# Kernel tuning notes

Measured on AMD Instinct MI355X. Metric: run time of the kernel, lower is better.

## Reference

```python
import jax, jax.numpy as jnp
import numpy as np

DIM_MODEL = 1024
DIM_K = 64
DIM_V = 64
H = 16
B = 2
S = 2048


def setup_inputs() -> dict:
    key = jax.random.key(0)
    ks = jax.random.split(key, 11)
    s = 0.02
    return {
        "Q": jax.random.normal(ks[0], (B, S, DIM_MODEL), jnp.float32),
        "K": jax.random.normal(ks[1], (B, S, DIM_MODEL), jnp.float32),
        "V": jax.random.normal(ks[2], (B, S, DIM_MODEL), jnp.float32),
        "Wq": jax.random.normal(ks[3], (DIM_MODEL, H * DIM_K), jnp.float32) * s,
        "bq": jnp.zeros((H * DIM_K,), jnp.float32),
        "Wk": jax.random.normal(ks[4], (DIM_MODEL, H * DIM_K), jnp.float32) * s,
        "bk": jnp.zeros((H * DIM_K,), jnp.float32),
        "Wv": jax.random.normal(ks[5], (DIM_MODEL, H * DIM_V), jnp.float32) * s,
        "bv": jnp.zeros((H * DIM_V,), jnp.float32),
        "Wo": jax.random.normal(ks[6], (H * DIM_V, DIM_MODEL), jnp.float32) * s,
        "bo": jnp.zeros((DIM_MODEL,), jnp.float32),
    }


def reference(Q, K, V, Wq, bq, Wk, bk, Wv, bv, Wo, bo):
    b, len_q = Q.shape[0], Q.shape[1]
    # QKV projections, split heads: [b, h, S, d]
    q = (Q @ Wq + bq).reshape(b, len_q, H, DIM_K).transpose(0, 2, 1, 3)
    k = (K @ Wk + bk).reshape(b, K.shape[1], H, DIM_K).transpose(0, 2, 1, 3)
    v = (V @ Wv + bv).reshape(b, V.shape[1], H, DIM_V).transpose(0, 2, 1, 3)
    # FAITHFUL QUIRK: original scales by sqrt(K.shape[0]) == batch size, not dim_k
    scale = 1.0 / np.sqrt(b).astype(np.float32)
    att = jnp.einsum('bhqd,bhkd->bhqk', q * scale, k)
    att = jax.nn.softmax(att, axis=-1)
    out = jnp.einsum('bhqk,bhkd->bhqd', att, v)  # [b,h,S,dv]
    out = out.transpose(0, 2, 1, 3).reshape(b, len_q, H * DIM_V)
    return out @ Wo + bo
```

## Files before the change

### kernel.cpp

```cpp
#include <hip/hip_runtime.h>
#include <hip/hip_bf16.h>


using bf16 = __hip_bfloat16;
typedef __attribute__((ext_vector_type(4))) float f32x4;
typedef __attribute__((ext_vector_type(8))) short bf16x8;

__device__ __forceinline__ void gload_lds16(const void* gsrc, void* ldst) {
    __builtin_amdgcn_global_load_lds(
        (const __attribute__((address_space(1))) void*)gsrc,
        (__attribute__((address_space(3))) void*)ldst,
        16, 0, 0);
}

__device__ __forceinline__ float fexp2(float x) {
    float r; asm("v_exp_f32 %0, %1" : "=v"(r) : "v"(x)); return r;
}

__device__ __forceinline__ unsigned cvtpk(float a, float b) {
    unsigned d; asm("v_cvt_pk_bf16_f32 %0, %1, %2" : "=v"(d) : "v"(a), "v"(b));
    return d;
}

__device__ __forceinline__ void pls32(unsigned &a, unsigned &b) {
    asm("v_permlane32_swap_b32 %0, %1" : "+v"(a), "+v"(b));
}
__device__ __forceinline__ void pls16(unsigned &a, unsigned &b) {
    asm("v_permlane16_swap_b32 %0, %1" : "+v"(a), "+v"(b));
}

__device__ __forceinline__ unsigned pack2bf(float a, float b) {
    unsigned short ua = __builtin_bit_cast(unsigned short, __float2bfloat16(a));
    unsigned short ub = __builtin_bit_cast(unsigned short, __float2bfloat16(b));
    return (unsigned)ua | ((unsigned)ub << 16);
}

__global__ void prep_kernel(const float* __restrict__ X0, const float* __restrict__ X1,
                            const float* __restrict__ X2,
                            bf16* __restrict__ O0, bf16* __restrict__ O1, bf16* __restrict__ O2,
                            const float* __restrict__ W0, const float* __restrict__ W1,
                            const float* __restrict__ W2, const float* __restrict__ W3,
                            bf16* __restrict__ T0, bf16* __restrict__ T1,
                            bf16* __restrict__ T2, bf16* __restrict__ T3,
                            int n4) {
    const int z = blockIdx.z;
    if (z < 3) {
        const float* in = z == 0 ? X0 : (z == 1 ? X1 : X2);
        bf16* out = z == 0 ? O0 : (z == 1 ? O1 : O2);
        int idx = blockIdx.x * blockDim.x + threadIdx.x;
        int stride = gridDim.x * blockDim.x;
        for (int i = idx; i < n4; i += stride) {
            float4 v = reinterpret_cast<const float4*>(in)[i];
            reinterpret_cast<uint2*>(out)[i] = make_uint2(pack2bf(v.x, v.y), pack2bf(v.z, v.w));
        }
    } else {
        const int w = z - 3;
        const float* W = w == 0 ? W0 : (w == 1 ? W1 : (w == 2 ? W2 : W3));
        bf16* WT = w == 0 ? T0 : (w == 1 ? T1 : (w == 2 ? T2 : T3));
        __shared__ float t[32][33];
        int bx = (blockIdx.x & 31) * 32, by = (blockIdx.x >> 5) * 32;
        int x = threadIdx.x & 31, y = threadIdx.x >> 5;
        #pragma unroll
        for (int i = 0; i < 4; ++i)
            t[y + 8*i][x] = W[(size_t)(by + y + 8*i) * 1024 + bx + x];
        __syncthreads();
        #pragma unroll
        for (int i = 0; i < 4; ++i)
            WT[(size_t)(bx + y + 8*i) * 1024 + by + x] = __float2bfloat16(t[x][y + 8*i]);
    }
}

template<int NTILE>
__global__ __launch_bounds__(256, (NTILE == 128) ? 2 : 3)
void gemm_bt(const bf16* __restrict__ A0, const bf16* __restrict__ A1, const bf16* __restrict__ A2,
             const bf16* __restrict__ B0, const bf16* __restrict__ B1, const bf16* __restrict__ B2,
             const float* __restrict__ bi0, const float* __restrict__ bi1, const float* __restrict__ bi2,
             void* __restrict__ O0, void* __restrict__ O1, void* __restrict__ O2,
             int mode_base)
{
    const int f = blockIdx.x;
    int x, y, z;
    if (NTILE == 128) {
        const int s = f >> 3;
        y = s & 7;
        const int t = (f & 7) + 8 * (s >> 3);
        x = t & 31; z = t >> 5;
    } else {
        const int s = f >> 3;
        y = s & 15;
        x = (f & 7) + 8 * (s >> 4);
        z = 0;
    }
    const bf16* A  = z == 0 ? A0 : (z == 1 ? A1 : A2);
    const bf16* BT = z == 0 ? B0 : (z == 1 ? B1 : B2);
    const float* bias = z == 0 ? bi0 : (z == 1 ? bi1 : bi2);
    void* Cout = z == 0 ? O0 : (z == 1 ? O1 : O2);
    const int mode = mode_base + z;

    constexpr int ABYTES = 16384;
    constexpr int BBYTES = NTILE * 128;
    constexpr int BUFB   = ABYTES + BBYTES;
    __shared__ __align__(16) char Sbuf[2 * BUFB];
    constexpr int MF = (NTILE == 128) ? 4 : 2;
    const int tid = threadIdx.x;
    const int wave = tid >> 6, lane = tid & 63;
    const int g = lane >> 4, ln = lane & 15;
    const int m0 = x * 128, n0 = y * NTILE;
    const int wm = (NTILE == 128) ? (wave >> 1) * 64 : wave * 32;
    const int wn = (NTILE == 128) ? (wave & 1) * 64 : 0;
    const int lnsw = (ln & 7) << 4;

    auto stage = [&](int k0, int buf) {
        char* Ab = Sbuf + buf * BUFB;
        char* Bb = Ab + ABYTES;
        #pragma unroll
        for (int rd = 0; rd < 4; ++rd) {
            int row = rd * 32 + (tid >> 3);
            int src = ((tid & 7) * 16) ^ (((tid >> 3) & 7) << 4);
            gload_lds16((const char*)(A + (size_t)(m0 + row) * 1024 + k0) + src,
                        Ab + rd * 4096 + tid * 16);
        }
        #pragma unroll
        for (int rd = 0; rd < NTILE / 32; ++rd) {
            int row = rd * 32 + (tid >> 3);
            int src = ((tid & 7) * 16) ^ (((tid >> 3) & 7) << 4);
            gload_lds16((const char*)(BT + (size_t)(n0 + row) * 1024 + k0) + src,
                        Bb + rd * 4096 + tid * 16);
        }
    };

    f32x4 acc[MF][4] = {};
    stage(0, 0);

    for (int k = 0; k < 16; ++k) {
        const int cur = k & 1;
        asm volatile("s_waitcnt vmcnt(0)\n\ts_barrier" ::: "memory");
        __builtin_amdgcn_sched_barrier(0);
        if (k < 15) stage((k + 1) * 64, cur ^ 1);
        __builtin_amdgcn_sched_barrier(0);

        const char* Ab = Sbuf + cur * BUFB;
        const char* Bb = Ab + ABYTES;
        #pragma unroll
        for (int kk = 0; kk < 2; ++kk) {
            bf16x8 af[MF], bfr[4];
            #pragma unroll
            for (int mf = 0; mf < MF; ++mf)
                af[mf] = *(const bf16x8*)(Ab + (wm + mf*16 + ln) * 128 + ((kk*64 + g*16) ^ lnsw));
            #pragma unroll
            for (int nf = 0; nf < 4; ++nf)
                bfr[nf] = *(const bf16x8*)(Bb + (wn + nf*16 + ln) * 128 + ((kk*64 + g*16) ^ lnsw));
            #pragma unroll
            for (int mf = 0; mf < MF; ++mf)
                #pragma unroll
                for (int nf = 0; nf < 4; ++nf)
                    acc[mf][nf] = __builtin_amdgcn_mfma_f32_16x16x32_bf16(af[mf], bfr[nf], acc[mf][nf], 0, 0, 0);
        }
    }

    const float scl = (mode == 0) ? (0.70710678118654752f * 1.44269504088896340f) : 1.0f;

    if (mode == 2) {
        #pragma unroll
        for (int mf = 0; mf < MF; ++mf) {
            #pragma unroll
            for (int nf = 0; nf < 4; ++nf) {
                int col = n0 + wn + nf*16 + ln;
                float bv = bias[col];
                int row0 = m0 + wm + mf*16 + g*4;
                int b = row0 >> 11, ss = row0 & 2047;
                int hh = col >> 6, dv = col & 63;
                bf16* dst = (bf16*)Cout + (((size_t)(b*16 + hh) * 64 + dv) << 11) + ss;
                *(uint2*)dst = make_uint2(
                    pack2bf(acc[mf][nf][0] + bv, acc[mf][nf][1] + bv),
                    pack2bf(acc[mf][nf][2] + bv, acc[mf][nf][3] + bv));
            }
        }
    } else if (mode == 0 || mode == 1) {
        __syncthreads();
        #pragma unroll
        for (int mf = 0; mf < MF; ++mf) {
            #pragma unroll
            for (int nf = 0; nf < 4; ++nf) {
                int tcol = wn + nf*16 + ln;
                float bv = bias[n0 + tcol];
                #pragma unroll
                for (int r = 0; r < 4; ++r) {
                    int trow = wm + mf*16 + g*4 + r;
                    *(unsigned short*)(Sbuf + trow * (NTILE*2) + tcol * 2) =
                        __builtin_bit_cast(unsigned short,
                            __float2bfloat16((acc[mf][nf][r] + bv) * scl));
                }
            }
        }
        __syncthreads();
        constexpr int TPR = NTILE / 8;
        const int rr = tid / TPR, cc = (tid % TPR) * 8;
        #pragma unroll
        for (int it = 0; it < 128 / (256 / TPR); ++it) {
            int row = it * (256 / TPR) + rr;
            uint4 v = *(const uint4*)(Sbuf + row * (NTILE*2) + cc * 2);
            *(uint4*)((bf16*)Cout + (size_t)(m0 + row) * 1024 + n0 + cc) = v;
        }
    } else {
        #pragma unroll
        for (int p = 0; p < 2; ++p) {
            __syncthreads();
            #pragma unroll
            for (int mf = 0; mf < MF; ++mf) {
                #pragma unroll
                for (int j = 0; j < 2; ++j) {
                    int nf = p * 2 + j;
                    int tcol = j*16 + ln;
                    float bv = bias[n0 + wn + nf*16 + ln];
                    #pragma unroll
                    for (int r = 0; r < 4; ++r) {
                        int trow = wm + mf*16 + g*4 + r;
                        *(float*)(Sbuf + trow * 128 + tcol * 4) = acc[mf][nf][r] + bv;
                    }
                }
            }
            __syncthreads();
            const int rr = tid >> 3, cc = (tid & 7) * 4;
            #pragma unroll
            for (int it = 0; it < 4; ++it) {
                int row = it * 32 + rr;
                uint4 v = *(const uint4*)(Sbuf + row * 128 + cc * 4);
                *(uint4*)((float*)Cout + (size_t)(m0 + row) * 1024 + n0 + p*32 + cc) = v;
            }
        }
    }
}

__global__ __launch_bounds__(256, 2)
void attn_kernel(const bf16* __restrict__ qh, const bf16* __restrict__ kh,
                 const bf16* __restrict__ vt, bf16* __restrict__ aout)
{
    __shared__ __align__(16) bf16 Kls[2][128 * 64];
    __shared__ __align__(16) bf16 Vls[2][64 * 128];
    const int f = blockIdx.x;
    const int xcd = f & 7, s = f >> 3, i = s & 15, ghi = s >> 4;
    const int bh = xcd + 8 * ghi;
    const int b = bh >> 4, h = bh & 15;
    const int q0 = i * 128;

    const int tid = threadIdx.x;
    const int wave = tid >> 6, lane = tid & 63;
    const int g = lane >> 4, ln = lane & 15;
    const int srow = lane >> 3;
    const int scol = ((lane & 7) * 16) ^ ((srow & 7) << 4);
    const int lnsw = (ln & 7) << 4;

    const bf16* kbase = kh + (size_t)(b * 2048) * 1024 + h * 64;
    const bf16* vbase = vt + (size_t)bh * 64 * 2048;

    const int vrow_in = lane >> 4;
    const int vcol16 = lane & 15;

    bf16x8 qf[2][2];
    #pragma unroll
    for (int nf = 0; nf < 2; ++nf) {
        const bf16* qrow = qh + (size_t)(b*2048 + q0 + wave*32 + nf*16 + ln) * 1024 + h*64;
        qf[nf][0] = *(const bf16x8*)(qrow + g*8);
        qf[nf][1] = *(const bf16x8*)(qrow + 32 + g*8);
    }

    auto stageKV = [&](int kv0, int buf) {
        #pragma unroll
        for (int c2 = 0; c2 < 4; ++c2) {
            int c = wave * 4 + c2;
            int krow = c * 8 + srow;
            gload_lds16((const char*)(kbase + (size_t)(kv0 + krow) * 1024) + scol,
                        (char*)&Kls[buf][0] + c * 1024);
        }
        #pragma unroll
        for (int c2 = 0; c2 < 4; ++c2) {
            int c = wave * 4 + c2;
            int vrow = c * 4 + vrow_in;
            int sc16 = vcol16 ^ (vrow & 15);
            gload_lds16((const char*)(vbase + (size_t)vrow * 2048 + kv0) + sc16 * 16,
                        (char*)&Vls[buf][0] + c * 1024);
        }
    };

    stageKV(0, 0);

    f32x4 oacc[4][2] = {};
    f32x4 lacc[2] = {};
    union PU { unsigned u[4]; bf16x8 v; };
    PU ones;
    ones.u[0] = ones.u[1] = ones.u[2] = ones.u[3] = 0x3F803F80u;

    for (int t = 0; t < 16; ++t) {
        const int cur = t & 1;
        asm volatile("s_waitcnt vmcnt(0)\n\ts_barrier" ::: "memory");
        __builtin_amdgcn_sched_barrier(0);
        if (t < 15) stageKV((t + 1) * 128, cur ^ 1);
        __builtin_amdgcn_sched_barrier(0);

        const char* Kc = (const char*)&Kls[cur][0];
        const char* Vc = (const char*)&Vls[cur][0];

        f32x4 sacA[4][2] = {}, sacB[4][2] = {};
        __builtin_amdgcn_s_setprio(1);
        #pragma unroll
        for (int kk = 0; kk < 2; ++kk) {
            bf16x8 kf[4];
            #pragma unroll
            for (int mf = 0; mf < 4; ++mf)
                kf[mf] = *(const bf16x8*)(Kc + (mf*16 + ln) * 128 + ((kk*64 + g*16) ^ lnsw));
            #pragma unroll
            for (int mf = 0; mf < 4; ++mf)
                #pragma unroll
                for (int nf = 0; nf < 2; ++nf)
                    sacA[mf][nf] = __builtin_amdgcn_mfma_f32_16x16x32_bf16(kf[mf], qf[nf][kk], sacA[mf][nf], 0, 0, 0);
        }
        #pragma unroll
        for (int kk = 0; kk < 2; ++kk) {
            bf16x8 kf[4];
            #pragma unroll
            for (int mf = 0; mf < 4; ++mf)
                kf[mf] = *(const bf16x8*)(Kc + (64 + mf*16 + ln) * 128 + ((kk*64 + g*16) ^ lnsw));
            #pragma unroll
            for (int mf = 0; mf < 4; ++mf)
                #pragma unroll
                for (int nf = 0; nf < 2; ++nf)
                    sacB[mf][nf] = __builtin_amdgcn_mfma_f32_16x16x32_bf16(kf[mf], qf[nf][kk], sacB[mf][nf], 0, 0, 0);
        }
        __builtin_amdgcn_s_setprio(0);

        PU pfh[2][2][2];
        #pragma unroll
        for (int ha = 0; ha < 2; ++ha) {
            f32x4 (&sac)[4][2] = ha ? sacB : sacA;
            #pragma unroll
            for (int nf = 0; nf < 2; ++nf) {
                unsigned w[4][2];
                #pragma unroll
                for (int mf = 0; mf < 4; ++mf) {
                    float e0 = fexp2(sac[mf][nf][0]);
                    float e1 = fexp2(sac[mf][nf][1]);
                    float e2 = fexp2(sac[mf][nf][2]);
                    float e3 = fexp2(sac[mf][nf][3]);
                    w[mf][0] = cvtpk(e0, e1);
                    w[mf][1] = cvtpk(e2, e3);
                }
                #pragma unroll
                for (int kk = 0; kk < 2; ++kk) {
                    #pragma unroll
                    for (int rp = 0; rp < 2; ++rp) {
                        unsigned a = w[2*kk][rp], bb = w[2*kk + 1][rp];
                        pls32(a, bb);
                        pls16(a, bb);
                        pfh[ha][nf][kk].u[rp] = a;
                        pfh[ha][nf][kk].u[2 + rp] = bb;
                    }
                }
            }
        }

        __builtin_amdgcn_s_setprio(1);
        #pragma unroll
        for (int ha = 0; ha < 2; ++ha) {
            #pragma unroll
            for (int kk = 0; kk < 2; ++kk) {
                bf16x8 vf[4];
                #pragma unroll
                for (int mf = 0; mf < 4; ++mf)
                    vf[mf] = *(const bf16x8*)(Vc + (mf*16 + ln) * 256 + (((ha*8 + kk*4 + g) ^ ln) << 4));
                #pragma unroll
                for (int nf = 0; nf < 2; ++nf)
                    lacc[nf] = __builtin_amdgcn_mfma_f32_16x16x32_bf16(ones.v, pfh[ha][nf][kk].v, lacc[nf], 0, 0, 0);
                #pragma unroll
                for (int mf = 0; mf < 4; ++mf)
                    #pragma unroll
                    for (int nf = 0; nf < 2; ++nf)
                        oacc[mf][nf] = __builtin_amdgcn_mfma_f32_16x16x32_bf16(vf[mf], pfh[ha][nf][kk].v, oacc[mf][nf], 0, 0, 0);
            }
        }
        __builtin_amdgcn_s_setprio(0);
    }

    #pragma unroll
    for (int nf = 0; nf < 2; ++nf) {
        float inv = 1.0f / lacc[nf][0];
        int q = q0 + wave*32 + nf*16 + ln;
        bf16* orow = aout + (size_t)(b*2048 + q) * 1024 + h * 64;
        #pragma unroll
        for (int mf = 0; mf < 4; ++mf) {
            *(uint2*)(orow + mf*16 + g*4) = make_uint2(
                pack2bf(oacc[mf][nf][0] * inv, oacc[mf][nf][1] * inv),
                pack2bf(oacc[mf][nf][2] * inv, oacc[mf][nf][3] * inv));
        }
    }
}

extern "C" void kernel_launch(void* const* d_in, const int* in_sizes, int n_in,
                              void* d_out, int out_size, void* d_ws, size_t ws_size,
                              hipStream_t stream)
{
    const float* Q  = (const float*)d_in[0];
    const float* K  = (const float*)d_in[1];
    const float* V  = (const float*)d_in[2];
    const float* Wq = (const float*)d_in[3];
    const float* bq = (const float*)d_in[4];
    const float* Wk = (const float*)d_in[5];
    const float* bk = (const float*)d_in[6];
    const float* Wv = (const float*)d_in[7];
    const float* bv = (const float*)d_in[8];
    const float* Wo = (const float*)d_in[9];
    const float* bo = (const float*)d_in[10];

    char* ws = (char*)d_ws;
    const size_t MB = 1024 * 1024;
    bf16* Qbf  = (bf16*)(ws + 0);
    bf16* Kbf  = (bf16*)(ws + 8*MB);
    bf16* Vbf  = (bf16*)(ws + 16*MB);
    bf16* WqT  = (bf16*)(ws + 24*MB);
    bf16* WkT  = (bf16*)(ws + 26*MB);
    bf16* WvT  = (bf16*)(ws + 28*MB);
    bf16* WoT  = (bf16*)(ws + 30*MB);
    bf16* qhp  = (bf16*)(ws + 32*MB);
    bf16* khp  = (bf16*)(ws + 40*MB);
    bf16* vtp  = (bf16*)(ws + 48*MB);
    bf16* aout = (bf16*)(ws + 0);

    const int n4 = (2 * 2048 * 1024) / 4;
    prep_kernel<<<dim3(1024, 1, 7), 256, 0, stream>>>(Q, K, V, Qbf, Kbf, Vbf,
                                                      Wq, Wk, Wv, Wo, WqT, WkT, WvT, WoT, n4);

    gemm_bt<128><<<768, 256, 0, stream>>>(Qbf, Kbf, Vbf, WqT, WkT, WvT,
                                          bq, bk, bv, qhp, khp, vtp, 0);

    attn_kernel<<<512, 256, 0, stream>>>(qhp, khp, vtp, aout);

    gemm_bt<64><<<512, 256, 0, stream>>>(aout, aout, aout, WoT, WoT, WoT,
                                         bo, bo, bo, d_out, d_out, d_out, 3);
}
```

Before: 104.4 us.

## Load V fragments directly from global into registers instead of LDS staging

Drops the double-buffered V tile in LDS. Each wave now reads its V MFMA operands straight from global memory into registers at the start of every KV iteration, issued before the next K tile is staged. This halves LDS use, which may allow more blocks per CU, and removes the LDS reads for V. In exchange every wave re-fetches the same V tile from global/L2 with no sharing across waves. The loads are not prefetched a tile ahead, so their latency can sit on the critical path, and the vmcnt(0) wait also covers them. Register pressure rises by 16 bf16x8 values per lane.

```diff
diff --git a/kernel.cpp b/kernel.cpp
--- a/kernel.cpp
+++ b/kernel.cpp
@@ -237,7 +237,6 @@
                  const bf16* __restrict__ vt, bf16* __restrict__ aout)
 {
     __shared__ __align__(16) bf16 Kls[2][128 * 64];
-    __shared__ __align__(16) bf16 Vls[2][64 * 128];
     const int f = blockIdx.x;
     const int xcd = f & 7, s = f >> 3, i = s & 15, ghi = s >> 4;
     const int bh = xcd + 8 * ghi;
@@ -254,9 +253,6 @@
     const bf16* kbase = kh + (size_t)(b * 2048) * 1024 + h * 64;
     const bf16* vbase = vt + (size_t)bh * 64 * 2048;
 
-    const int vrow_in = lane >> 4;
-    const int vcol16 = lane & 15;
-
     bf16x8 qf[2][2];
     #pragma unroll
     for (int nf = 0; nf < 2; ++nf) {
@@ -265,7 +261,7 @@
         qf[nf][1] = *(const bf16x8*)(qrow + 32 + g*8);
     }
 
-    auto stageKV = [&](int kv0, int buf) {
+    auto stageK = [&](int kv0, int buf) {
         #pragma unroll
         for (int c2 = 0; c2 < 4; ++c2) {
             int c = wave * 4 + c2;
@@ -273,17 +269,9 @@
             gload_lds16((const char*)(kbase + (size_t)(kv0 + krow) * 1024) + scol,
                         (char*)&Kls[buf][0] + c * 1024);
         }
-        #pragma unroll
-        for (int c2 = 0; c2 < 4; ++c2) {
-            int c = wave * 4 + c2;
-            int vrow = c * 4 + vrow_in;
-            int sc16 = vcol16 ^ (vrow & 15);
-            gload_lds16((const char*)(vbase + (size_t)vrow * 2048 + kv0) + sc16 * 16,
-                        (char*)&Vls[buf][0] + c * 1024);
-        }
     };
 
-    stageKV(0, 0);
+    stageK(0, 0);
 
     f32x4 oacc[4][2] = {};
     f32x4 lacc[2] = {};
@@ -291,15 +279,30 @@
     PU ones;
     ones.u[0] = ones.u[1] = ones.u[2] = ones.u[3] = 0x3F803F80u;
 
+    const bf16* vrow[4];
+    #pragma unroll
+    for (int mf = 0; mf < 4; ++mf)
+        vrow[mf] = vbase + (size_t)(mf*16 + ln) * 2048;
+
     for (int t = 0; t < 16; ++t) {
         const int cur = t & 1;
         asm volatile("s_waitcnt vmcnt(0)\n\ts_barrier" ::: "memory");
         __builtin_amdgcn_sched_barrier(0);
-        if (t < 15) stageKV((t + 1) * 128, cur ^ 1);
+
+        bf16x8 vreg[2][2][4];
+        const int kv0 = t * 128;
+        #pragma unroll
+        for (int ha = 0; ha < 2; ++ha)
+            #pragma unroll
+            for (int kk = 0; kk < 2; ++kk)
+                #pragma unroll
+                for (int mf = 0; mf < 4; ++mf)
+                    vreg[ha][kk][mf] = *(const bf16x8*)(vrow[mf] + kv0 + (ha*8 + kk*4 + g) * 8);
+
+        if (t < 15) stageK((t + 1) * 128, cur ^ 1);
         __builtin_amdgcn_sched_barrier(0);
 
         const char* Kc = (const char*)&Kls[cur][0];
-        const char* Vc = (const char*)&Vls[cur][0];
 
         f32x4 sacA[4][2] = {}, sacB[4][2] = {};
         __builtin_amdgcn_s_setprio(1);
@@ -364,10 +367,6 @@
         for (int ha = 0; ha < 2; ++ha) {
             #pragma unroll
             for (int kk = 0; kk < 2; ++kk) {
-                bf16x8 vf[4];
-                #pragma unroll
-                for (int mf = 0; mf < 4; ++mf)
-                    vf[mf] = *(const bf16x8*)(Vc + (mf*16 + ln) * 256 + (((ha*8 + kk*4 + g) ^ ln) << 4));
                 #pragma unroll
                 for (int nf = 0; nf < 2; ++nf)
                     lacc[nf] = __builtin_amdgcn_mfma_f32_16x16x32_bf16(ones.v, pfh[ha][nf][kk].v, lacc[nf], 0, 0, 0);
@@ -375,7 +374,7 @@
                 for (int mf = 0; mf < 4; ++mf)
                     #pragma unroll
                     for (int nf = 0; nf < 2; ++nf)
-                        oacc[mf][nf] = __builtin_amdgcn_mfma_f32_16x16x32_bf16(vf[mf], pfh[ha][nf][kk].v, oacc[mf][nf], 0, 0, 0);
+                        oacc[mf][nf] = __builtin_amdgcn_mfma_f32_16x16x32_bf16(vreg[ha][kk][mf], pfh[ha][nf][kk].v, oacc[mf][nf], 0, 0, 0);
             }
         }
         __builtin_amdgcn_s_setprio(0);
```

Result: slower. 131.4 us (+25.9%).
